# Performance work log

Measured on AMD Instinct MI355X. Metric: run time of the kernel, lower is better.

Reference implementation:

```python
import jax, jax.numpy as jnp
import numpy as np

N0, N1, N2 = 120000, 40000, 10000   # sampled node counts per hop
E0, E1 = 600000, 150000             # edges per block (fanout ~15)
DIN, DH, NC = 128, 256, 47


def _glorot(k, fan_in, fan_out):
    s = (2.0 / (fan_in + fan_out)) ** 0.5
    return jax.random.normal(k, (fan_in, fan_out), jnp.float32) * s


def setup_inputs() -> dict:
    key = jax.random.key(0)
    ks = jax.random.split(key, 20)
    x0 = jax.random.normal(ks[0], (N0, DIN), jnp.float32)
    src0 = jax.random.randint(ks[1], (E0,), 0, N0)
    dst0 = jax.random.randint(ks[2], (E0,), 0, N1)
    src1 = jax.random.randint(ks[3], (E1,), 0, N1)
    dst1 = jax.random.randint(ks[4], (E1,), 0, N2)
    srcb0 = jax.random.randint(ks[5], (E0,), 0, N0)
    dstb0 = jax.random.randint(ks[6], (E0,), 0, N1)
    srcb1 = jax.random.randint(ks[7], (E1,), 0, N1)
    dstb1 = jax.random.randint(ks[8], (E1,), 0, N2)
    # id_old_value_new: must satisfy idx[:n] < n for every truncation length n,
    # i.e. idx[k] in [0, k+1)
    rng = np.random.default_rng(0)
    idx = jnp.asarray((rng.random(N0) * (np.arange(N0) + 1)).astype(np.int64))
    mix_ratio = jnp.float32(0.5)
    Wl0 = _glorot(ks[9], DIN, DH); Wr0 = _glorot(ks[10], DIN, DH)
    b0 = jnp.zeros((DH,), jnp.float32)
    Wl1 = _glorot(ks[11], DH, DH); Wr1 = _glorot(ks[12], DH, DH)
    b1 = jnp.zeros((DH,), jnp.float32)
    Wlin = _glorot(ks[13], DH, NC)
    blin = jnp.zeros((NC,), jnp.float32)
    return dict(x0=x0, src0=src0, dst0=dst0, src1=src1, dst1=dst1,
                srcb0=srcb0, dstb0=dstb0, srcb1=srcb1, dstb1=dstb1,
                idx=idx, mix_ratio=mix_ratio,
                Wl0=Wl0, Wr0=Wr0, b0=b0, Wl1=Wl1, Wr1=Wr1, b1=b1,
                Wlin=Wlin, blin=blin)


def _sage(x_all, root_x, src, dst, n_root, Wl, Wr, b):
    # PyG-style SAGEConv, mean aggregation: lin_l(mean_j x_j) + lin_r(root)
    msgs = x_all[src]                                        # [E, D] gather
    s = jax.ops.segment_sum(msgs, dst, num_segments=n_root)  # [n_root, D]
    cnt = jax.ops.segment_sum(jnp.ones_like(dst, dtype=x_all.dtype), dst,
                              num_segments=n_root)
    mean = s / jnp.maximum(cnt, 1.0)[:, None]
    return mean @ Wl + root_x @ Wr + b


def reference(x0, src0, dst0, src1, dst1, srcb0, dstb0, srcb1, dstb1,
              idx, mix_ratio, Wl0, Wr0, b0, Wl1, Wr1, b1, Wlin, blin):
    blocks = [(src0, dst0, N1), (src1, dst1, N2)]
    blocks_b = [(srcb0, dstb0, N1), (srcb1, dstb1, N2)]
    params = [(Wl0, Wr0, b0), (Wl1, Wr1, b1)]
    m = mix_ratio

    # first branch (dropout omitted: inference mode)
    aggr_xs = [x0]
    for i in range(2):
        src, dst, n_root = blocks[i]
        Wl, Wr, b = params[i]
        root_x = aggr_xs[-1][:n_root]
        x = jax.nn.relu(_sage(aggr_xs[-1], root_x, src, dst, n_root, Wl, Wr, b))
        aggr_xs.append(x)

    # permuted branch via id_old_value_new gather
    aggr_xs_b = [x[idx[: x.shape[0]]] for x in aggr_xs]

    x_mix = aggr_xs[0] * m + aggr_xs_b[0] * (1.0 - m)
    for i in range(2):
        src, dst, n_root = blocks[i]
        srcb, dstb, n_root_b = blocks_b[i]
        Wl, Wr, b = params[i]
        x_new = jax.nn.relu(_sage(aggr_xs[i], x_mix[:n_root], src, dst,
                                  n_root, Wl, Wr, b))
        x_new_b = jax.nn.relu(_sage(aggr_xs_b[i], x_mix[:n_root_b], srcb, dstb,
                                    n_root_b, Wl, Wr, b))
        x_mix = x_new * m + x_new_b * (1.0 - m)

    logits = x_mix @ Wlin + blin
    return jax.nn.log_softmax(logits, axis=-1)
```

## Files before the change

### kernel.cpp

```cpp
#include <hip/hip_runtime.h>
#include <math.h>

#define N1C 40000
#define N2C 10000
#define DIN 128
#define DH  256
#define NC  47

#define TOTCNT (2 * N1C + 2 * N2C)
#define CAP 64

typedef __attribute__((ext_vector_type(8))) short v8s;
typedef __attribute__((ext_vector_type(4))) float v4f;
typedef __attribute__((ext_vector_type(2))) float v2f;

#if __has_builtin(__builtin_amdgcn_cvt_pk_f32_fp8)
#define HW_FP8 1
#endif

__device__ __forceinline__ unsigned short f2bf(float f) {
    unsigned int u = __float_as_uint(f);
    u += 0x7FFF + ((u >> 16) & 1);
    return (unsigned short)(u >> 16);
}
__device__ __forceinline__ float bf2f(unsigned int h) {
    return __uint_as_float(h << 16);
}

__device__ __forceinline__ unsigned char f2e4m3(float f) {
    unsigned int u = __float_as_uint(f);
    unsigned char s = (unsigned char)((u >> 24) & 0x80);
    float a = __uint_as_float(u & 0x7FFFFFFF);
    if (a > 448.0f) a = 448.0f;
    if (a < 0.015625f) {
        int k = (int)rintf(a * 512.0f);
        return s | (unsigned char)k;
    }
    unsigned int bits = __float_as_uint(a);
    int et = (int)(bits >> 23) - 127 + 7;
    unsigned int m32 = bits & 0x7FFFFF;
    unsigned int m3 = m32 >> 20;
    unsigned int rest = m32 & 0xFFFFF;
    if (rest > 0x80000 || (rest == 0x80000 && (m3 & 1))) m3++;
    if (m3 == 8) { m3 = 0; et++; }
    if (et > 15 || (et == 15 && m3 == 7)) return s | 0x7E;
    return s | (unsigned char)((et << 3) | m3);
}

#ifndef HW_FP8
__device__ __forceinline__ void build_lut(float* lut, int t) {
    if (t < 256) {
        int e = (t >> 3) & 15, mm = t & 7;
        float d = (e == 0) ? (float)mm * (1.0f / 512.0f)
                           : (1.0f + (float)mm * 0.125f) * exp2f((float)(e - 7));
        if (t & 0x80) d = -d;
        lut[t] = d;
    }
}
#endif

__device__ __forceinline__ void dec4(unsigned int u, float& f0, float& f1,
                                     float& f2, float& f3, const float* lut) {
#ifdef HW_FP8
    v2f lo = __builtin_amdgcn_cvt_pk_f32_fp8((int)u, false);
    v2f hi = __builtin_amdgcn_cvt_pk_f32_fp8((int)u, true);
    f0 = lo[0]; f1 = lo[1]; f2 = hi[0]; f3 = hi[1];
#else
    f0 = lut[u & 0xFF]; f1 = lut[(u >> 8) & 0xFF];
    f2 = lut[(u >> 16) & 0xFF]; f3 = lut[u >> 24];
#endif
}

__global__ __launch_bounds__(256) void front_fused(
        const int* __restrict__ src0, const int* __restrict__ dst0,
        const int* __restrict__ srcb0, const int* __restrict__ dstb0,
        const int* __restrict__ src1, const int* __restrict__ dst1,
        const int* __restrict__ srcb1, const int* __restrict__ dstb1,
        const int* __restrict__ perm, int* __restrict__ cur,
        int* __restrict__ bucket, int E0, int E1, int nbFill,
        const float* __restrict__ x0, unsigned char* __restrict__ x0f,
        long n8, int nbConv,
        const float* __restrict__ Wl0, const float* __restrict__ Wr0,
        const float* __restrict__ Wl1, const float* __restrict__ Wr1,
        unsigned short* __restrict__ Wt0l, unsigned short* __restrict__ Wt0r,
        unsigned short* __restrict__ Wt1l, unsigned short* __restrict__ Wt1r) {
    int b = blockIdx.x, t = threadIdx.x;
    if (b < nbFill) {
        int e = b * 256 + t;
        int tot = 2 * E0 + 2 * E1;
        if (e >= tot) return;
        int s, bin;
        if (e < E0) {
            s = src0[e];                  bin = dst0[e];
        } else if (e < 2 * E0) {
            int le = e - E0;
            s = perm[srcb0[le]];          bin = N1C + dstb0[le];
        } else if (e < 2 * E0 + E1) {
            int le = e - 2 * E0;
            s = src1[le];                 bin = 2 * N1C + dst1[le];
        } else {
            int le = e - 2 * E0 - E1;
            s = perm[srcb1[le]];          bin = 2 * N1C + N2C + dstb1[le];
        }
        int pos = atomicAdd(&cur[bin], 1);
        if (pos < CAP) bucket[(size_t)bin * CAP + pos] = s;
    } else if (b < nbFill + nbConv) {
        long i = (long)(b - nbFill) * 256 + t;
        if (i >= n8) return;
        const float4* p = (const float4*)(x0 + i * 8);
        float4 a = p[0], c = p[1];
        float f[8] = {a.x, a.y, a.z, a.w, c.x, c.y, c.z, c.w};
        unsigned int q0 = 0, q1 = 0;
#pragma unroll
        for (int j = 0; j < 8; j++) {
            unsigned int e8 = f2e4m3(f[j]);
            if (j < 4) q0 |= e8 << (8 * j); else q1 |= e8 << (8 * (j - 4));
        }
        uint2 q = {q0, q1};
        *(uint2*)(x0f + i * 8) = q;
    } else {
        int id = (b - nbFill - nbConv) * 256 + t;
        const int S0 = DIN * DH;
        const int S1 = DH * DH;
        const float* W; unsigned short* Wt; int K, loc;
        if (id < S0)                   { W = Wl0; Wt = Wt0l; K = DIN; loc = id; }
        else if (id < 2 * S0)          { W = Wr0; Wt = Wt0r; K = DIN; loc = id - S0; }
        else if (id < 2 * S0 + S1)     { W = Wl1; Wt = Wt1l; K = DH;  loc = id - 2 * S0; }
        else if (id < 2 * S0 + 2 * S1) { W = Wr1; Wt = Wt1r; K = DH;  loc = id - 2 * S0 - S1; }
        else return;
        int n = loc / K, k = loc - n * K;
        Wt[(size_t)n * K + k] = f2bf(W[(size_t)k * DH + n]);
    }
}

__global__ __launch_bounds__(256) void gather_mean_128f(
        const unsigned char* __restrict__ xf, const int* __restrict__ bucket,
        const int* __restrict__ cur, unsigned short* __restrict__ mean0,
        unsigned short* __restrict__ meanb0) {
#ifndef HW_FP8
    __shared__ float lutm[256];
    build_lut(lutm, threadIdx.x);
    __syncthreads();
    const float* lut = lutm;
#else
    const float* lut = nullptr;
#endif
    const int half = N1C / 8;
    int b = blockIdx.x;
    int binbase; unsigned short* outp; int rb;
    if (b < half) { binbase = 0;   outp = mean0;  rb = b; }
    else          { binbase = N1C; outp = meanb0; rb = b - half; }
    int wv = threadIdx.x >> 6, lane = threadIdx.x & 63;
    int row = rb * 8 + wv * 2 + (lane >> 5);
    int c4 = (lane & 31) * 4;
    int bin = binbase + row;
    int cnt = min(cur[bin], CAP);
    const int* cs = bucket + (size_t)bin * CAP;
    float a0 = 0.0f, a1 = 0.0f, a2 = 0.0f, a3 = 0.0f;
    int i = 0;
    for (; i + 1 < cnt; i += 2) {
        int s0 = cs[i], s1 = cs[i + 1];
        unsigned int u = *(const unsigned int*)&xf[(size_t)s0 * DIN + c4];
        unsigned int v = *(const unsigned int*)&xf[(size_t)s1 * DIN + c4];
        float u0, u1, u2, u3, w0, w1, w2, w3;
        dec4(u, u0, u1, u2, u3, lut);
        dec4(v, w0, w1, w2, w3, lut);
        a0 += u0 + w0; a1 += u1 + w1; a2 += u2 + w2; a3 += u3 + w3;
    }
    if (i < cnt) {
        unsigned int u = *(const unsigned int*)&xf[(size_t)cs[i] * DIN + c4];
        float u0, u1, u2, u3;
        dec4(u, u0, u1, u2, u3, lut);
        a0 += u0; a1 += u1; a2 += u2; a3 += u3;
    }
    float inv = 1.0f / (float)max(cnt, 1);
    uint2 o;
    o.x = (unsigned int)f2bf(a0 * inv) | ((unsigned int)f2bf(a1 * inv) << 16);
    o.y = (unsigned int)f2bf(a2 * inv) | ((unsigned int)f2bf(a3 * inv) << 16);
    *(uint2*)&outp[(size_t)row * DIN + c4] = o;
}

__global__ __launch_bounds__(256) void gather_mean_256f(
        const unsigned char* __restrict__ xf, const int* __restrict__ bucket,
        const int* __restrict__ cur, unsigned short* __restrict__ mean1,
        unsigned short* __restrict__ meanb1) {
#ifndef HW_FP8
    __shared__ float lutm[256];
    build_lut(lutm, threadIdx.x);
    __syncthreads();
    const float* lut = lutm;
#else
    const float* lut = nullptr;
#endif
    const int half = N2C / 4;
    int b = blockIdx.x;
    int binbase; unsigned short* outp; int rb;
    if (b < half) { binbase = 2 * N1C;       outp = mean1;  rb = b; }
    else          { binbase = 2 * N1C + N2C; outp = meanb1; rb = b - half; }
    int row = rb * 4 + (threadIdx.x >> 6);
    int lane = threadIdx.x & 63;
    int bin = binbase + row;
    int cnt = min(cur[bin], CAP);
    const int* cs = bucket + (size_t)bin * CAP;
    float a0 = 0.0f, a1 = 0.0f, a2 = 0.0f, a3 = 0.0f;
    int i = 0;
    for (; i + 1 < cnt; i += 2) {
        int s0 = cs[i], s1 = cs[i + 1];
        unsigned int u = *(const unsigned int*)&xf[(size_t)s0 * DH + lane * 4];
        unsigned int v = *(const unsigned int*)&xf[(size_t)s1 * DH + lane * 4];
        float u0, u1, u2, u3, w0, w1, w2, w3;
        dec4(u, u0, u1, u2, u3, lut);
        dec4(v, w0, w1, w2, w3, lut);
        a0 += u0 + w0; a1 += u1 + w1; a2 += u2 + w2; a3 += u3 + w3;
    }
    if (i < cnt) {
        unsigned int u = *(const unsigned int*)&xf[(size_t)cs[i] * DH + lane * 4];
        float u0, u1, u2, u3;
        dec4(u, u0, u1, u2, u3, lut);
        a0 += u0; a1 += u1; a2 += u2; a3 += u3;
    }
    float inv = 1.0f / (float)max(cnt, 1);
    uint2 o;
    o.x = (unsigned int)f2bf(a0 * inv) | ((unsigned int)f2bf(a1 * inv) << 16);
    o.y = (unsigned int)f2bf(a2 * inv) | ((unsigned int)f2bf(a3 * inv) << 16);
    *(uint2*)&outp[(size_t)row * DH + lane * 4] = o;
}

#define KP0 136
#define H0T 5
__global__ __launch_bounds__(256, 2) void hop0_mfma(
        const float* __restrict__ x0, const int* __restrict__ idx,
        const unsigned short* __restrict__ mean0, const unsigned short* __restrict__ meanb0,
        const unsigned short* __restrict__ Wtl, const unsigned short* __restrict__ Wtr,
        const float* __restrict__ b, const float* __restrict__ mixp,
        unsigned char* __restrict__ x1f, unsigned short* __restrict__ xm1) {
    __shared__ unsigned short Alds[4][16][KP0];
    int t = threadIdx.x;
    int wv = t >> 6, lane = t & 63;
    int mrow = lane & 15, quad = lane >> 4;
    float m = *mixp;

    v8s wl[4][4], wr[4][4];
    float bb[4];
#pragma unroll
    for (int ct = 0; ct < 4; ct++) {
        int n = wv * 64 + ct * 16 + mrow;
        bb[ct] = b[n];
#pragma unroll
        for (int ks = 0; ks < 4; ks++) {
            int k0 = ks * 32 + quad * 8;
            wl[ct][ks] = *(const v8s*)&Wtl[(size_t)n * DIN + k0];
            wr[ct][ks] = *(const v8s*)&Wtr[(size_t)n * DIN + k0];
        }
    }

    for (int tile = 0; tile < H0T; tile++) {
        int row0 = (blockIdx.x * H0T + tile) * 16;
        {
            int r = t >> 4, k0 = (t & 15) * 8;
            int rg = row0 + r;
            *(v8s*)&Alds[0][r][k0] = *(const v8s*)&mean0[(size_t)rg * DIN + k0];
            *(v8s*)&Alds[1][r][k0] = *(const v8s*)&meanb0[(size_t)rg * DIN + k0];
            const float4* xr4 = (const float4*)&x0[(size_t)rg * DIN + k0];
            float4 A0 = xr4[0], A1 = xr4[1];
            int ib = idx[rg];
            const float4* xb4 = (const float4*)&x0[(size_t)ib * DIN + k0];
            float4 B0 = xb4[0], B1 = xb4[1];
            float fa[8] = {A0.x, A0.y, A0.z, A0.w, A1.x, A1.y, A1.z, A1.w};
            float fb[8] = {B0.x, B0.y, B0.z, B0.w, B1.x, B1.y, B1.z, B1.w};
            v8s vr, vm;
#pragma unroll
            for (int j = 0; j < 8; j++) {
                vr[j] = (short)f2bf(fa[j]);
                vm[j] = (short)f2bf(m * fa[j] + (1.0f - m) * fb[j]);
            }
            *(v8s*)&Alds[2][r][k0] = vr;
            *(v8s*)&Alds[3][r][k0] = vm;
        }
        __syncthreads();
        v4f accA[4], accB[4], accC[4], accD[4];
#pragma unroll
        for (int ct = 0; ct < 4; ct++) {
            accA[ct] = (v4f){0.f, 0.f, 0.f, 0.f}; accB[ct] = (v4f){0.f, 0.f, 0.f, 0.f};
            accC[ct] = (v4f){0.f, 0.f, 0.f, 0.f}; accD[ct] = (v4f){0.f, 0.f, 0.f, 0.f};
        }
#pragma unroll
        for (int ks = 0; ks < 4; ks++) {
            int k0 = ks * 32 + quad * 8;
            v8s aM = *(v8s*)&Alds[0][mrow][k0];
            v8s aB = *(v8s*)&Alds[1][mrow][k0];
            v8s aR = *(v8s*)&Alds[2][mrow][k0];
            v8s aX = *(v8s*)&Alds[3][mrow][k0];
#pragma unroll
            for (int ct = 0; ct < 4; ct++) {
                accA[ct] = __builtin_amdgcn_mfma_f32_16x16x32_bf16(aM, wl[ct][ks], accA[ct], 0, 0, 0);
                accB[ct] = __builtin_amdgcn_mfma_f32_16x16x32_bf16(aB, wl[ct][ks], accB[ct], 0, 0, 0);
                accC[ct] = __builtin_amdgcn_mfma_f32_16x16x32_bf16(aR, wr[ct][ks], accC[ct], 0, 0, 0);
                accD[ct] = __builtin_amdgcn_mfma_f32_16x16x32_bf16(aX, wr[ct][ks], accD[ct], 0, 0, 0);
            }
        }
#pragma unroll
        for (int ct = 0; ct < 4; ct++) {
            int col = wv * 64 + ct * 16 + mrow;
#pragma unroll
            for (int r = 0; r < 4; r++) {
                int row = row0 + quad * 4 + r;
                float pA = accA[ct][r], pB = accB[ct][r], pC = accC[ct][r], pD = accD[ct][r];
                float xv  = fmaxf(pA + pC + bb[ct], 0.0f);
                float xn  = fmaxf(pA + pD + bb[ct], 0.0f);
                float xnb = fmaxf(pB + pD + bb[ct], 0.0f);
                x1f[(size_t)row * DH + col] = f2e4m3(xv);
                xm1[(size_t)row * DH + col] = f2bf(m * xn + (1.0f - m) * xnb);
            }
        }
        __syncthreads();
    }
}

#define KP1 264
#define H1T 2
__global__ __launch_bounds__(256, 2) void hop1_mfma(
        const unsigned short* __restrict__ mean1, const unsigned short* __restrict__ meanb1,
        const unsigned short* __restrict__ xm1,
        const unsigned short* __restrict__ Wtl, const unsigned short* __restrict__ Wtr,
        const float* __restrict__ b, const float* __restrict__ mixp,
        float* __restrict__ xm2) {
    __shared__ unsigned short Alds[3][16][KP1];
    int t = threadIdx.x;
    int wv = t >> 6, lane = t & 63;
    int mrow = lane & 15, quad = lane >> 4;
    float m = *mixp;

    v8s wlc[4][4], wrc[4][4];
    float bb[4];
#pragma unroll
    for (int ct = 0; ct < 4; ct++) {
        int n = wv * 64 + ct * 16 + mrow;
        bb[ct] = b[n];
#pragma unroll
        for (int ks = 0; ks < 4; ks++) {
            int k0 = ks * 32 + quad * 8;
            wlc[ct][ks] = *(const v8s*)&Wtl[(size_t)n * DH + k0];
            wrc[ct][ks] = *(const v8s*)&Wtr[(size_t)n * DH + k0];
        }
    }

    for (int tt = 0; tt < H1T; tt++) {
        int tIdx = blockIdx.x * H1T + tt;
        if (tIdx >= N2C / 16) break;
        int row0 = tIdx * 16;
        {
            int r = t >> 4, k0 = (t & 15) * 16;
            int rg = row0 + r;
            *(v8s*)&Alds[0][r][k0]     = *(const v8s*)&mean1[(size_t)rg * DH + k0];
            *(v8s*)&Alds[0][r][k0 + 8] = *(const v8s*)&mean1[(size_t)rg * DH + k0 + 8];
            *(v8s*)&Alds[1][r][k0]     = *(const v8s*)&meanb1[(size_t)rg * DH + k0];
            *(v8s*)&Alds[1][r][k0 + 8] = *(const v8s*)&meanb1[(size_t)rg * DH + k0 + 8];
            *(v8s*)&Alds[2][r][k0]     = *(const v8s*)&xm1[(size_t)rg * DH + k0];
            *(v8s*)&Alds[2][r][k0 + 8] = *(const v8s*)&xm1[(size_t)rg * DH + k0 + 8];
        }
        __syncthreads();
        v4f accA[4], accB[4], accC[4];
#pragma unroll
        for (int ct = 0; ct < 4; ct++) {
            accA[ct] = (v4f){0.f, 0.f, 0.f, 0.f};
            accB[ct] = (v4f){0.f, 0.f, 0.f, 0.f};
            accC[ct] = (v4f){0.f, 0.f, 0.f, 0.f};
        }
#pragma unroll
        for (int ks = 0; ks < 8; ks++) {
            int k0 = ks * 32 + quad * 8;
            v8s aM = *(v8s*)&Alds[0][mrow][k0];
            v8s aB = *(v8s*)&Alds[1][mrow][k0];
            v8s aR = *(v8s*)&Alds[2][mrow][k0];
#pragma unroll
            for (int ct = 0; ct < 4; ct++) {
                v8s bl, br;
                if (ks < 4) { bl = wlc[ct][ks]; br = wrc[ct][ks]; }
                else {
                    int n = wv * 64 + ct * 16 + mrow;
                    bl = *(const v8s*)&Wtl[(size_t)n * DH + k0];
                    br = *(const v8s*)&Wtr[(size_t)n * DH + k0];
                }
                accA[ct] = __builtin_amdgcn_mfma_f32_16x16x32_bf16(aM, bl, accA[ct], 0, 0, 0);
                accB[ct] = __builtin_amdgcn_mfma_f32_16x16x32_bf16(aB, bl, accB[ct], 0, 0, 0);
                accC[ct] = __builtin_amdgcn_mfma_f32_16x16x32_bf16(aR, br, accC[ct], 0, 0, 0);
            }
        }
#pragma unroll
        for (int ct = 0; ct < 4; ct++) {
            int col = wv * 64 + ct * 16 + mrow;
#pragma unroll
            for (int r = 0; r < 4; r++) {
                int row = row0 + quad * 4 + r;
                float xn  = fmaxf(accA[ct][r] + accC[ct][r] + bb[ct], 0.0f);
                float xnb = fmaxf(accB[ct][r] + accC[ct][r] + bb[ct], 0.0f);
                xm2[(size_t)row * DH + col] = m * xn + (1.0f - m) * xnb;
            }
        }
        __syncthreads();
    }
}

__global__ __launch_bounds__(256) void logits_lsm(
        const float* __restrict__ xmix2, const float* __restrict__ Wlin,
        const float* __restrict__ blin, float* __restrict__ out, int nrows) {
    int w = threadIdx.x >> 6;
    int row = blockIdx.x * 4 + w;
    if (row >= nrows) return;
    int t = threadIdx.x & 63;
    __shared__ float xs[4][DH];
    for (int i = t; i < DH; i += 64) xs[w][i] = xmix2[(size_t)row * DH + i];
    __builtin_amdgcn_s_waitcnt(0);
    float acc = 0.0f;
    if (t < NC) {
        acc = blin[t];
        for (int k = 0; k < DH; k++) acc += xs[w][k] * Wlin[k * NC + t];
    }
    float v = (t < NC) ? acc : -INFINITY;
    float mx = v;
    for (int off = 32; off; off >>= 1) mx = fmaxf(mx, __shfl_xor(mx, off, 64));
    float ex = (t < NC) ? expf(acc - mx) : 0.0f;
    float sum = ex;
    for (int off = 32; off; off >>= 1) sum += __shfl_xor(sum, off, 64);
    if (t < NC) out[(size_t)row * NC + t] = acc - mx - logf(sum);
}

extern "C" void kernel_launch(void* const* d_in, const int* in_sizes, int n_in,
                              void* d_out, int out_size, void* d_ws, size_t ws_size,
                              hipStream_t stream) {
    const float* x0    = (const float*)d_in[0];
    const int*   src0  = (const int*)d_in[1];
    const int*   dst0  = (const int*)d_in[2];
    const int*   src1  = (const int*)d_in[3];
    const int*   dst1  = (const int*)d_in[4];
    const int*   srcb0 = (const int*)d_in[5];
    const int*   dstb0 = (const int*)d_in[6];
    const int*   srcb1 = (const int*)d_in[7];
    const int*   dstb1 = (const int*)d_in[8];
    const int*   idx   = (const int*)d_in[9];
    const float* mixp  = (const float*)d_in[10];
    const float* Wl0   = (const float*)d_in[11];
    const float* Wr0   = (const float*)d_in[12];
    const float* b0    = (const float*)d_in[13];
    const float* Wl1   = (const float*)d_in[14];
    const float* Wr1   = (const float*)d_in[15];
    const float* b1    = (const float*)d_in[16];
    const float* Wlin  = (const float*)d_in[17];
    const float* blin  = (const float*)d_in[18];
    float* out = (float*)d_out;

    const int E0 = in_sizes[1];
    const int E1 = in_sizes[3];
    const long x0elems = (long)in_sizes[0];

    int* wsi    = (int*)d_ws;
    int* cur    = wsi;
    int* bucket = cur + TOTCNT;
    unsigned short* wsh = (unsigned short*)(bucket + (size_t)TOTCNT * CAP);
    unsigned short* mean0  = wsh;
    unsigned short* meanb0 = mean0  + (size_t)N1C * DIN;
    unsigned short* mean1  = meanb0 + (size_t)N1C * DIN;
    unsigned short* meanb1 = mean1  + (size_t)N2C * DH;
    unsigned short* xm1h   = meanb1 + (size_t)N2C * DH;
    unsigned short* Wt0l   = xm1h   + (size_t)N1C * DH;
    unsigned short* Wt0r   = Wt0l + DIN * DH;
    unsigned short* Wt1l   = Wt0r + DIN * DH;
    unsigned short* Wt1r   = Wt1l + DH * DH;
    float* xm2 = (float*)(Wt1r + DH * DH);
    unsigned char* x0f = (unsigned char*)(xm2 + (size_t)N2C * DH);
    unsigned char* x1f = x0f + (size_t)x0elems;

    hipMemsetAsync(cur, 0, sizeof(int) * TOTCNT, stream);

    int etot = 2 * E0 + 2 * E1;
    int nbFill = (etot + 255) / 256;
    long n8 = x0elems / 8;
    int nbConv = (int)((n8 + 255) / 256);
    int nbW = (2 * DIN * DH + 2 * DH * DH + 255) / 256;
    front_fused<<<nbFill + nbConv + nbW, 256, 0, stream>>>(
        src0, dst0, srcb0, dstb0, src1, dst1, srcb1, dstb1, idx, cur, bucket,
        E0, E1, nbFill, x0, x0f, n8, nbConv,
        Wl0, Wr0, Wl1, Wr1, Wt0l, Wt0r, Wt1l, Wt1r);

    gather_mean_128f<<<2 * (N1C / 8), 256, 0, stream>>>(x0f, bucket, cur, mean0, meanb0);

    hop0_mfma<<<N1C / (16 * H0T), 256, 0, stream>>>(x0, idx, mean0, meanb0, Wt0l, Wt0r,
                                                    b0, mixp, x1f, xm1h);

    gather_mean_256f<<<2 * (N2C / 4), 256, 0, stream>>>(x1f, bucket, cur, mean1, meanb1);

    hop1_mfma<<<(N2C / 16 + H1T - 1) / H1T, 256, 0, stream>>>(mean1, meanb1, xm1h,
                                                              Wt1l, Wt1r, b1, mixp, xm2);

    logits_lsm<<<(N2C + 3) / 4, 256, 0, stream>>>(xm2, Wlin, blin, out, N2C);
}
```

Baseline: 366.3 us.

## Fuse neighbor mean-gather into hop MFMA kernels, drop intermediate mean buffers

The separate gather_mean kernels for both hops are removed. Each hop kernel now computes the FP8 neighbor means for its own 16-row tile and writes them as bf16 straight into shared memory before the MFMA stage. This saves two kernel launches and the global write and reread of the mean buffers. In exchange, the irregular gathers now run inside blocks with fewer resident waves (launch bounds 256,2, and the hop1 grid is small), which can hurt latency hiding. The non-hardware FP8 path also switches from a shared-memory lookup table to per-byte arithmetic decoding.

```diff
diff --git a/kernel.cpp b/kernel.cpp
--- a/kernel.cpp
+++ b/kernel.cpp
@@ -47,27 +47,21 @@
     return s | (unsigned char)((et << 3) | m3);
 }
 
-#ifndef HW_FP8
-__device__ __forceinline__ void build_lut(float* lut, int t) {
-    if (t < 256) {
-        int e = (t >> 3) & 15, mm = t & 7;
-        float d = (e == 0) ? (float)mm * (1.0f / 512.0f)
-                           : (1.0f + (float)mm * 0.125f) * exp2f((float)(e - 7));
-        if (t & 0x80) d = -d;
-        lut[t] = d;
-    }
-}
-#endif
-
 __device__ __forceinline__ void dec4(unsigned int u, float& f0, float& f1,
-                                     float& f2, float& f3, const float* lut) {
+                                     float& f2, float& f3) {
 #ifdef HW_FP8
     v2f lo = __builtin_amdgcn_cvt_pk_f32_fp8((int)u, false);
     v2f hi = __builtin_amdgcn_cvt_pk_f32_fp8((int)u, true);
     f0 = lo[0]; f1 = lo[1]; f2 = hi[0]; f3 = hi[1];
 #else
-    f0 = lut[u & 0xFF]; f1 = lut[(u >> 8) & 0xFF];
-    f2 = lut[(u >> 16) & 0xFF]; f3 = lut[u >> 24];
+    auto d1 = [](unsigned int b) -> float {
+        int e = (b >> 3) & 15, mm = b & 7;
+        float d = (e == 0) ? (float)mm * (1.0f / 512.0f)
+                           : (1.0f + (float)mm * 0.125f) * exp2f((float)(e - 7));
+        return (b & 0x80) ? -d : d;
+    };
+    f0 = d1(u & 0xFF); f1 = d1((u >> 8) & 0xFF);
+    f2 = d1((u >> 16) & 0xFF); f3 = d1(u >> 24);
 #endif
 }
 
@@ -133,104 +127,12 @@
     }
 }
 
-__global__ __launch_bounds__(256) void gather_mean_128f(
-        const unsigned char* __restrict__ xf, const int* __restrict__ bucket,
-        const int* __restrict__ cur, unsigned short* __restrict__ mean0,
-        unsigned short* __restrict__ meanb0) {
-#ifndef HW_FP8
-    __shared__ float lutm[256];
-    build_lut(lutm, threadIdx.x);
-    __syncthreads();
-    const float* lut = lutm;
-#else
-    const float* lut = nullptr;
-#endif
-    const int half = N1C / 8;
-    int b = blockIdx.x;
-    int binbase; unsigned short* outp; int rb;
-    if (b < half) { binbase = 0;   outp = mean0;  rb = b; }
-    else          { binbase = N1C; outp = meanb0; rb = b - half; }
-    int wv = threadIdx.x >> 6, lane = threadIdx.x & 63;
-    int row = rb * 8 + wv * 2 + (lane >> 5);
-    int c4 = (lane & 31) * 4;
-    int bin = binbase + row;
-    int cnt = min(cur[bin], CAP);
-    const int* cs = bucket + (size_t)bin * CAP;
-    float a0 = 0.0f, a1 = 0.0f, a2 = 0.0f, a3 = 0.0f;
-    int i = 0;
-    for (; i + 1 < cnt; i += 2) {
-        int s0 = cs[i], s1 = cs[i + 1];
-        unsigned int u = *(const unsigned int*)&xf[(size_t)s0 * DIN + c4];
-        unsigned int v = *(const unsigned int*)&xf[(size_t)s1 * DIN + c4];
-        float u0, u1, u2, u3, w0, w1, w2, w3;
-        dec4(u, u0, u1, u2, u3, lut);
-        dec4(v, w0, w1, w2, w3, lut);
-        a0 += u0 + w0; a1 += u1 + w1; a2 += u2 + w2; a3 += u3 + w3;
-    }
-    if (i < cnt) {
-        unsigned int u = *(const unsigned int*)&xf[(size_t)cs[i] * DIN + c4];
-        float u0, u1, u2, u3;
-        dec4(u, u0, u1, u2, u3, lut);
-        a0 += u0; a1 += u1; a2 += u2; a3 += u3;
-    }
-    float inv = 1.0f / (float)max(cnt, 1);
-    uint2 o;
-    o.x = (unsigned int)f2bf(a0 * inv) | ((unsigned int)f2bf(a1 * inv) << 16);
-    o.y = (unsigned int)f2bf(a2 * inv) | ((unsigned int)f2bf(a3 * inv) << 16);
-    *(uint2*)&outp[(size_t)row * DIN + c4] = o;
-}
-
-__global__ __launch_bounds__(256) void gather_mean_256f(
-        const unsigned char* __restrict__ xf, const int* __restrict__ bucket,
-        const int* __restrict__ cur, unsigned short* __restrict__ mean1,
-        unsigned short* __restrict__ meanb1) {
-#ifndef HW_FP8
-    __shared__ float lutm[256];
-    build_lut(lutm, threadIdx.x);
-    __syncthreads();
-    const float* lut = lutm;
-#else
-    const float* lut = nullptr;
-#endif
-    const int half = N2C / 4;
-    int b = blockIdx.x;
-    int binbase; unsigned short* outp; int rb;
-    if (b < half) { binbase = 2 * N1C;       outp = mean1;  rb = b; }
-    else          { binbase = 2 * N1C + N2C; outp = meanb1; rb = b - half; }
-    int row = rb * 4 + (threadIdx.x >> 6);
-    int lane = threadIdx.x & 63;
-    int bin = binbase + row;
-    int cnt = min(cur[bin], CAP);
-    const int* cs = bucket + (size_t)bin * CAP;
-    float a0 = 0.0f, a1 = 0.0f, a2 = 0.0f, a3 = 0.0f;
-    int i = 0;
-    for (; i + 1 < cnt; i += 2) {
-        int s0 = cs[i], s1 = cs[i + 1];
-        unsigned int u = *(const unsigned int*)&xf[(size_t)s0 * DH + lane * 4];
-        unsigned int v = *(const unsigned int*)&xf[(size_t)s1 * DH + lane * 4];
-        float u0, u1, u2, u3, w0, w1, w2, w3;
-        dec4(u, u0, u1, u2, u3, lut);
-        dec4(v, w0, w1, w2, w3, lut);
-        a0 += u0 + w0; a1 += u1 + w1; a2 += u2 + w2; a3 += u3 + w3;
-    }
-    if (i < cnt) {
-        unsigned int u = *(const unsigned int*)&xf[(size_t)cs[i] * DH + lane * 4];
-        float u0, u1, u2, u3;
-        dec4(u, u0, u1, u2, u3, lut);
-        a0 += u0; a1 += u1; a2 += u2; a3 += u3;
-    }
-    float inv = 1.0f / (float)max(cnt, 1);
-    uint2 o;
-    o.x = (unsigned int)f2bf(a0 * inv) | ((unsigned int)f2bf(a1 * inv) << 16);
-    o.y = (unsigned int)f2bf(a2 * inv) | ((unsigned int)f2bf(a3 * inv) << 16);
-    *(uint2*)&outp[(size_t)row * DH + lane * 4] = o;
-}
-
 #define KP0 136
 #define H0T 5
-__global__ __launch_bounds__(256, 2) void hop0_mfma(
+__global__ __launch_bounds__(256, 2) void hop0_fused(
         const float* __restrict__ x0, const int* __restrict__ idx,
-        const unsigned short* __restrict__ mean0, const unsigned short* __restrict__ meanb0,
+        const unsigned char* __restrict__ x0f,
+        const int* __restrict__ bucket, const int* __restrict__ cur,
         const unsigned short* __restrict__ Wtl, const unsigned short* __restrict__ Wtr,
         const float* __restrict__ b, const float* __restrict__ mixp,
         unsigned char* __restrict__ x1f, unsigned short* __restrict__ xm1) {
@@ -254,13 +156,12 @@
         }
     }
 
+    int sub = lane >> 5, l32 = lane & 31, c4 = l32 * 4;
     for (int tile = 0; tile < H0T; tile++) {
         int row0 = (blockIdx.x * H0T + tile) * 16;
         {
             int r = t >> 4, k0 = (t & 15) * 8;
             int rg = row0 + r;
-            *(v8s*)&Alds[0][r][k0] = *(const v8s*)&mean0[(size_t)rg * DIN + k0];
-            *(v8s*)&Alds[1][r][k0] = *(const v8s*)&meanb0[(size_t)rg * DIN + k0];
             const float4* xr4 = (const float4*)&x0[(size_t)rg * DIN + k0];
             float4 A0 = xr4[0], A1 = xr4[1];
             int ib = idx[rg];
@@ -277,6 +178,36 @@
             *(v8s*)&Alds[2][r][k0] = vr;
             *(v8s*)&Alds[3][r][k0] = vm;
         }
+#pragma unroll
+        for (int it = 0; it < 4; it++) {
+            int h = it * 8 + wv * 2 + sub;
+            int row = h >> 1, br = h & 1;
+            int bin = (br ? N1C : 0) + row0 + row;
+            int cnt = min(cur[bin], CAP);
+            const int* cs = bucket + (size_t)bin * CAP;
+            float a0 = 0.f, a1 = 0.f, a2 = 0.f, a3 = 0.f;
+            int i = 0;
+            for (; i + 1 < cnt; i += 2) {
+                int s0 = cs[i], s1 = cs[i + 1];
+                unsigned int u = *(const unsigned int*)&x0f[(size_t)s0 * DIN + c4];
+                unsigned int v = *(const unsigned int*)&x0f[(size_t)s1 * DIN + c4];
+                float u0, u1, u2, u3, w0, w1, w2, w3;
+                dec4(u, u0, u1, u2, u3);
+                dec4(v, w0, w1, w2, w3);
+                a0 += u0 + w0; a1 += u1 + w1; a2 += u2 + w2; a3 += u3 + w3;
+            }
+            if (i < cnt) {
+                unsigned int u = *(const unsigned int*)&x0f[(size_t)cs[i] * DIN + c4];
+                float u0, u1, u2, u3;
+                dec4(u, u0, u1, u2, u3);
+                a0 += u0; a1 += u1; a2 += u2; a3 += u3;
+            }
+            float inv = 1.0f / (float)max(cnt, 1);
+            uint2 o;
+            o.x = (unsigned int)f2bf(a0 * inv) | ((unsigned int)f2bf(a1 * inv) << 16);
+            o.y = (unsigned int)f2bf(a2 * inv) | ((unsigned int)f2bf(a3 * inv) << 16);
+            *(uint2*)&Alds[br][row][c4] = o;
+        }
         __syncthreads();
         v4f accA[4], accB[4], accC[4], accD[4];
 #pragma unroll
@@ -319,8 +250,9 @@
 
 #define KP1 264
 #define H1T 2
-__global__ __launch_bounds__(256, 2) void hop1_mfma(
-        const unsigned short* __restrict__ mean1, const unsigned short* __restrict__ meanb1,
+__global__ __launch_bounds__(256, 2) void hop1_fused(
+        const unsigned char* __restrict__ x1f,
+        const int* __restrict__ bucket, const int* __restrict__ cur,
         const unsigned short* __restrict__ xm1,
         const unsigned short* __restrict__ Wtl, const unsigned short* __restrict__ Wtr,
         const float* __restrict__ b, const float* __restrict__ mixp,
@@ -352,12 +284,39 @@
         {
             int r = t >> 4, k0 = (t & 15) * 16;
             int rg = row0 + r;
-            *(v8s*)&Alds[0][r][k0]     = *(const v8s*)&mean1[(size_t)rg * DH + k0];
-            *(v8s*)&Alds[0][r][k0 + 8] = *(const v8s*)&mean1[(size_t)rg * DH + k0 + 8];
-            *(v8s*)&Alds[1][r][k0]     = *(const v8s*)&meanb1[(size_t)rg * DH + k0];
-            *(v8s*)&Alds[1][r][k0 + 8] = *(const v8s*)&meanb1[(size_t)rg * DH + k0 + 8];
             *(v8s*)&Alds[2][r][k0]     = *(const v8s*)&xm1[(size_t)rg * DH + k0];
             *(v8s*)&Alds[2][r][k0 + 8] = *(const v8s*)&xm1[(size_t)rg * DH + k0 + 8];
+        }
+#pragma unroll
+        for (int it = 0; it < 8; it++) {
+            int h = it * 4 + wv;
+            int row = h >> 1, br = h & 1;
+            int bin = 2 * N1C + (br ? N2C : 0) + row0 + row;
+            int cnt = min(cur[bin], CAP);
+            const int* cs = bucket + (size_t)bin * CAP;
+            int c4 = lane * 4;
+            float a0 = 0.f, a1 = 0.f, a2 = 0.f, a3 = 0.f;
+            int i = 0;
+            for (; i + 1 < cnt; i += 2) {
+                int s0 = cs[i], s1 = cs[i + 1];
+                unsigned int u = *(const unsigned int*)&x1f[(size_t)s0 * DH + c4];
+                unsigned int v = *(const unsigned int*)&x1f[(size_t)s1 * DH + c4];
+                float u0, u1, u2, u3, w0, w1, w2, w3;
+                dec4(u, u0, u1, u2, u3);
+                dec4(v, w0, w1, w2, w3);
+                a0 += u0 + w0; a1 += u1 + w1; a2 += u2 + w2; a3 += u3 + w3;
+            }
+            if (i < cnt) {
+                unsigned int u = *(const unsigned int*)&x1f[(size_t)cs[i] * DH + c4];
+                float u0, u1, u2, u3;
+                dec4(u, u0, u1, u2, u3);
+                a0 += u0; a1 += u1; a2 += u2; a3 += u3;
+            }
+            float inv = 1.0f / (float)max(cnt, 1);
+            uint2 o;
+            o.x = (unsigned int)f2bf(a0 * inv) | ((unsigned int)f2bf(a1 * inv) << 16);
+            o.y = (unsigned int)f2bf(a2 * inv) | ((unsigned int)f2bf(a3 * inv) << 16);
+            *(uint2*)&Alds[br][row][c4] = o;
         }
         __syncthreads();
         v4f accA[4], accB[4], accC[4];
@@ -375,16 +334,16 @@
             v8s aR = *(v8s*)&Alds[2][mrow][k0];
 #pragma unroll
             for (int ct = 0; ct < 4; ct++) {
-                v8s bl, br;
-                if (ks < 4) { bl = wlc[ct][ks]; br = wrc[ct][ks]; }
+                v8s bl, br2;
+                if (ks < 4) { bl = wlc[ct][ks]; br2 = wrc[ct][ks]; }
                 else {
                     int n = wv * 64 + ct * 16 + mrow;
-                    bl = *(const v8s*)&Wtl[(size_t)n * DH + k0];
-                    br = *(const v8s*)&Wtr[(size_t)n * DH + k0];
+                    bl  = *(const v8s*)&Wtl[(size_t)n * DH + k0];
+                    br2 = *(const v8s*)&Wtr[(size_t)n * DH + k0];
                 }
                 accA[ct] = __builtin_amdgcn_mfma_f32_16x16x32_bf16(aM, bl, accA[ct], 0, 0, 0);
                 accB[ct] = __builtin_amdgcn_mfma_f32_16x16x32_bf16(aB, bl, accB[ct], 0, 0, 0);
-                accC[ct] = __builtin_amdgcn_mfma_f32_16x16x32_bf16(aR, br, accC[ct], 0, 0, 0);
+                accC[ct] = __builtin_amdgcn_mfma_f32_16x16x32_bf16(aR, br2, accC[ct], 0, 0, 0);
             }
         }
 #pragma unroll
@@ -458,11 +417,7 @@
     int* cur    = wsi;
     int* bucket = cur + TOTCNT;
     unsigned short* wsh = (unsigned short*)(bucket + (size_t)TOTCNT * CAP);
-    unsigned short* mean0  = wsh;
-    unsigned short* meanb0 = mean0  + (size_t)N1C * DIN;
-    unsigned short* mean1  = meanb0 + (size_t)N1C * DIN;
-    unsigned short* meanb1 = mean1  + (size_t)N2C * DH;
-    unsigned short* xm1h   = meanb1 + (size_t)N2C * DH;
+    unsigned short* xm1h   = wsh;
     unsigned short* Wt0l   = xm1h   + (size_t)N1C * DH;
     unsigned short* Wt0r   = Wt0l + DIN * DH;
     unsigned short* Wt1l   = Wt0r + DIN * DH;
@@ -483,15 +438,11 @@
         E0, E1, nbFill, x0, x0f, n8, nbConv,
         Wl0, Wr0, Wl1, Wr1, Wt0l, Wt0r, Wt1l, Wt1r);
 
-    gather_mean_128f<<<2 * (N1C / 8), 256, 0, stream>>>(x0f, bucket, cur, mean0, meanb0);
-
-    hop0_mfma<<<N1C / (16 * H0T), 256, 0, stream>>>(x0, idx, mean0, meanb0, Wt0l, Wt0r,
-                                                    b0, mixp, x1f, xm1h);
-
-    gather_mean_256f<<<2 * (N2C / 4), 256, 0, stream>>>(x1f, bucket, cur, mean1, meanb1);
-
-    hop1_mfma<<<(N2C / 16 + H1T - 1) / H1T, 256, 0, stream>>>(mean1, meanb1, xm1h,
-                                                              Wt1l, Wt1r, b1, mixp, xm2);
+    hop0_fused<<<N1C / (16 * H0T), 256, 0, stream>>>(
+        x0, idx, x0f, bucket, cur, Wt0l, Wt0r, b0, mixp, x1f, xm1h);
+
+    hop1_fused<<<(N2C / 16 + H1T - 1) / H1T, 256, 0, stream>>>(
+        x1f, bucket, cur, xm1h, Wt1l, Wt1r, b1, mixp, xm2);
 
     logits_lsm<<<(N2C + 3) / 4, 256, 0, stream>>>(xm2, Wlin, blin, out, N2C);
 }
```

New measurement: 521.2 us. +42.3%, slower.
